# Optimization experiments

Hardware: AMD Instinct MI355X
Metric: run time of the kernel (lower is better)

Reference implementation:

```python
import jax, jax.numpy as jnp
import numpy as np

LEAK = 0.01
TEMP = 1.0
N_ORB = 1024
CTX = 32
N_ALPHA = 32
N_BETA = 32
B = 8192
EPS = 1e-20


def _leaky(x):
    return jnp.where(x >= 0, x, LEAK * x)


def _scorer_mlp(x, W1, b1, W2, b2, W3, b3):
    h = _leaky(x @ W1 + b1)
    h = _leaky(h @ W2 + b2)
    return h @ W3 + b3


def _gumbel_topk(logits, gumbel, k, temp):
    # successive-softmax subset relaxation (Plackett-Luce style)
    scores0 = logits + gumbel

    def step(carry, _):
        scores, khot = carry
        onehot = jax.nn.softmax(scores / temp, axis=-1)
        khot = khot + onehot
        scores = scores + jnp.log(jnp.maximum(1.0 - onehot, EPS))
        return (scores, khot), None

    (_, khot), _ = jax.lax.scan(step, (scores0, jnp.zeros_like(scores0)), None, length=k)
    return khot


def _soft_to_hard(soft, k):
    # straight-through: hard forward, soft backward
    idx = jax.lax.top_k(soft, k)[1]                      # (B, k)
    bidx = jnp.arange(soft.shape[0])[:, None]
    hard = jnp.zeros_like(soft).at[bidx, idx].set(1.0)
    return jax.lax.stop_gradient(hard - soft) + soft


def _lin_init(key, fan_in, fan_out):
    s = 1.0 / np.sqrt(fan_in)
    k1, k2 = jax.random.split(key)
    W = jax.random.uniform(k1, (fan_in, fan_out), minval=-s, maxval=s, dtype=jnp.float32)
    b = jax.random.uniform(k2, (fan_out,), minval=-s, maxval=s, dtype=jnp.float32)
    return W, b


def setup_inputs() -> dict:
    key = jax.random.key(0)
    ks = jax.random.split(key, 12)
    # alpha scorer: input = n_orb (baseline only, context_dim=0)
    W1a, b1a = _lin_init(ks[0], N_ORB, 128)
    W2a, b2a = _lin_init(ks[1], 128, 64)
    W3a, b3a = _lin_init(ks[2], 64, N_ORB)
    # beta scorer: context proj n_orb -> 32, input = n_orb + 32
    Wc, bc = _lin_init(ks[3], N_ORB, CTX)
    W1b, b1b = _lin_init(ks[4], N_ORB + CTX, 128)
    W2b, b2b = _lin_init(ks[5], 128, 64)
    W3b, b3b = _lin_init(ks[6], 64, N_ORB)
    baseline_a = jnp.zeros((N_ORB,), jnp.float32)
    baseline_b = jnp.zeros((N_ORB,), jnp.float32)
    # Gumbel noise: -log(-log(U))
    ua = jax.random.uniform(ks[7], (B, N_ORB), minval=1e-6, maxval=1.0 - 1e-6)
    ub = jax.random.uniform(ks[8], (B, N_ORB), minval=1e-6, maxval=1.0 - 1e-6)
    g_alpha = -jnp.log(-jnp.log(ua))
    g_beta = -jnp.log(-jnp.log(ub))
    return {
        "baseline_a": baseline_a, "W1a": W1a, "b1a": b1a, "W2a": W2a, "b2a": b2a,
        "W3a": W3a, "b3a": b3a,
        "baseline_b": baseline_b, "Wc": Wc, "bc": bc, "W1b": W1b, "b1b": b1b,
        "W2b": W2b, "b2b": b2b, "W3b": W3b, "b3b": b3b,
        "g_alpha": g_alpha, "g_beta": g_beta,
        "batch_size": B,
    }


def reference(baseline_a, W1a, b1a, W2a, b2a, W3a, b3a,
              baseline_b, Wc, bc, W1b, b1b, W2b, b2b, W3b, b3b,
              g_alpha, g_beta, batch_size):
    # --- alpha scoring (context_dim = 0) ---
    base_a = jnp.broadcast_to(baseline_a, (batch_size, N_ORB))
    alpha_logits = _scorer_mlp(base_a, W1a, b1a, W2a, b2a, W3a, b3a) + base_a
    alpha_soft = _gumbel_topk(alpha_logits, g_alpha, N_ALPHA, TEMP)
    alpha_config = _soft_to_hard(alpha_soft, N_ALPHA)          # (B, N_ORB)
    # --- beta scoring conditioned on alpha config ---
    base_b = jnp.broadcast_to(baseline_b, (batch_size, N_ORB))
    ctx = alpha_config @ Wc + bc                               # (B, 32)
    net_in = jnp.concatenate([base_b, ctx], axis=-1)
    beta_logits = _scorer_mlp(net_in, W1b, b1b, W2b, b2b, W3b, b3b) + base_b
    beta_soft = _gumbel_topk(beta_logits, g_beta, N_BETA, TEMP)
    beta_config = _soft_to_hard(beta_soft, N_BETA)
    return jnp.concatenate([alpha_config, beta_config], axis=-1)  # (B, num_sites)
```

## Files before the change

kernel.cpp:

```cpp
#include <hip/hip_runtime.h>
#include <hip/hip_bf16.h>
#include <float.h>

#define N_ORB 1024
#define KSEL 32
#define LEAK 0.01f
#define LOG2E 1.4426950408889634f

typedef float f32x2 __attribute__((ext_vector_type(2)));

__device__ __forceinline__ float leaky(float x) { return x >= 0.0f ? x : LEAK * x; }

__device__ __forceinline__ f32x2 pk_add(f32x2 a, f32x2 b) {
  f32x2 d;
  asm("v_pk_add_f32 %0, %1, %2" : "=v"(d) : "v"(a), "v"(b));
  return d;
}
__device__ __forceinline__ f32x2 pk_mul(f32x2 a, f32x2 b) {
  f32x2 d;
  asm("v_pk_mul_f32 %0, %1, %2" : "=v"(d) : "v"(a), "v"(b));
  return d;
}
__device__ __forceinline__ f32x2 pk_fma(f32x2 a, f32x2 b, f32x2 c) {
  f32x2 d;
  asm("v_pk_fma_f32 %0, %1, %2, %3" : "=v"(d) : "v"(a), "v"(b), "v"(c));
  return d;
}
__device__ __forceinline__ f32x2 pk_fma_clamp(f32x2 a, f32x2 b, f32x2 c) {
  f32x2 d;
  asm("v_pk_fma_f32 %0, %1, %2, %3 clamp" : "=v"(d) : "v"(a), "v"(b), "v"(c));
  return d;
}

template <int CTRL, int RM>
__device__ __forceinline__ int dpp0_i(int v) {
  return __builtin_amdgcn_update_dpp(0, v, CTRL, RM, 0xF, true);
}
template <int CTRL>
__device__ __forceinline__ float dpp_zero(float v) {
  return __int_as_float(
      __builtin_amdgcn_update_dpp(0, __float_as_int(v), CTRL, 0xF, 0xF, true));
}
__device__ __forceinline__ float rdlane(float v, int l) {
  return __int_as_float(__builtin_amdgcn_readlane(__float_as_int(v), l));
}

__device__ __forceinline__ float wave_sum64_dpp(float v) {
  v += dpp_zero<0x111>(v);
  v += dpp_zero<0x112>(v);
  v += dpp_zero<0x114>(v);
  v += dpp_zero<0x118>(v);
  v += dpp_zero<0x142>(v);
  v += dpp_zero<0x143>(v);
  return rdlane(v, 63);
}
__device__ __forceinline__ int wave_isum64(int v) {
  v += dpp0_i<0x111, 0xF>(v);
  v += dpp0_i<0x112, 0xF>(v);
  v += dpp0_i<0x114, 0xF>(v);
  v += dpp0_i<0x118, 0xF>(v);
  v += dpp0_i<0x142, 0xF>(v);
  v += dpp0_i<0x143, 0xF>(v);
  return __builtin_amdgcn_readlane(v, 63);
}
__device__ __forceinline__ int wave_iscan64(int v) {
  v += dpp0_i<0x111, 0xF>(v);
  v += dpp0_i<0x112, 0xF>(v);
  v += dpp0_i<0x114, 0xF>(v);
  v += dpp0_i<0x118, 0xF>(v);
  v += dpp0_i<0x142, 0xA>(v);
  v += dpp0_i<0x143, 0xC>(v);
  return v;
}

__device__ void run_chain2(f32x2 w[16], f32x2 kh[16]) {
#pragma unroll
  for (int i = 0; i < 16; ++i) kh[i] = f32x2{0.0f, 0.0f};
  const f32x2 onev = f32x2{1.0f, 1.0f};
  for (int it = 0; it < KSEL; ++it) {
    f32x2 t0 = pk_add(w[0], w[1]), t1 = pk_add(w[2], w[3]);
    f32x2 t2 = pk_add(w[4], w[5]), t3 = pk_add(w[6], w[7]);
    f32x2 t4 = pk_add(w[8], w[9]), t5 = pk_add(w[10], w[11]);
    f32x2 t6 = pk_add(w[12], w[13]), t7 = pk_add(w[14], w[15]);
    t0 = pk_add(t0, t1); t2 = pk_add(t2, t3);
    t4 = pk_add(t4, t5); t6 = pk_add(t6, t7);
    t0 = pk_add(t0, t2); t4 = pk_add(t4, t6);
    t0 = pk_add(t0, t4);
    float Z0 = wave_sum64_dpp(t0.x);
    float Z1 = wave_sum64_dpp(t0.y);
    Z0 = fmaxf(Z0, 1e-30f);
    Z1 = fmaxf(Z1, 1e-30f);
    float r0 = __builtin_amdgcn_rcpf(Z0);
    float r1 = __builtin_amdgcn_rcpf(Z1);
    float rZ0 = __builtin_fmaf(__builtin_fmaf(-Z0, r0, 1.0f), r0, r0);
    float rZ1 = __builtin_fmaf(__builtin_fmaf(-Z1, r1, 1.0f), r1, r1);
    const f32x2 rZ = f32x2{rZ0, rZ1};
    const f32x2 rZn = f32x2{-rZ0, -rZ1};
#pragma unroll
    for (int i = 0; i < 16; ++i) {
      kh[i] = pk_fma(w[i], rZ, kh[i]);
      f32x2 om = pk_fma_clamp(w[i], rZn, onev);
      w[i] = pk_mul(w[i], om);
    }
  }
}

__device__ unsigned tie_mask16(const f32x2 kh[16], bool comp_y, unsigned T,
                               int lane) {
  unsigned gt = 0, eq = 0;
#pragma unroll
  for (int i = 0; i < 16; ++i) {
    const unsigned u = __float_as_uint(comp_y ? kh[i].y : kh[i].x);
    gt |= (u > T ? 1u : 0u) << i;
    eq |= (u == T ? 1u : 0u) << i;
  }
  const int n_gt = wave_isum64(__popc(gt));
  const int m = 32 - n_gt;
  const int pe = __popc(eq);
  const int be = wave_iscan64(pe) - pe;
  int need = m - be;
  need = need < 0 ? 0 : (need > pe ? pe : need);
  unsigned tk = 0;
  unsigned em = eq;
  for (int guard = 0; guard < 16; ++guard) {
    if (!__any(need > 0)) break;
    if (need > 0) {
      const int bpos = __ffs(em) - 1;
      tk |= 1u << bpos;
      em &= em - 1;
      --need;
    }
  }
  return gt | tk;
}

__device__ void top32_mask2(const f32x2 kh[16], int lane, unsigned& m0,
                            unsigned& m1) {
  unsigned lo0 = 0, lo1 = 0;
  bool ex0 = false, ex1 = false;
  for (int b = 30; b >= 0; --b) {
    const unsigned c0v = lo0 | (1u << b);
    const unsigned c1v = lo1 | (1u << b);
    int c0 = 0, c1 = 0;
#pragma unroll
    for (int i = 0; i < 16; ++i) {
      c0 += __popcll(__ballot(__float_as_uint(kh[i].x) >= c0v));
      c1 += __popcll(__ballot(__float_as_uint(kh[i].y) >= c1v));
    }
    if (!ex0 && c0 >= 32) { lo0 = c0v; ex0 = (c0 == 32); }
    if (!ex1 && c1 >= 32) { lo1 = c1v; ex1 = (c1 == 32); }
    if (ex0 && ex1) break;
  }

  if (ex0) {
    unsigned mk = 0;
#pragma unroll
    for (int i = 0; i < 16; ++i)
      mk |= (__float_as_uint(kh[i].x) >= lo0 ? 1u : 0u) << i;
    m0 = mk;
  } else {
    m0 = tie_mask16(kh, false, lo0, lane);
  }
  if (ex1) {
    unsigned mk = 0;
#pragma unroll
    for (int i = 0; i < 16; ++i)
      mk |= (__float_as_uint(kh[i].y) >= lo1 ? 1u : 0u) << i;
    m1 = mk;
  } else {
    m1 = tie_mask16(kh, true, lo1, lane);
  }
}

__device__ __forceinline__ void compact_idx(unsigned mask, int lane,
                                            int* __restrict__ dst) {
  const int pe = __popc(mask);
  int base = wave_iscan64(pe) - pe;
  unsigned m = mask;
  while (m) {
    const int s = __ffs(m) - 1;
    m &= m - 1;
    dst[base++] = (lane << 4) | s;
  }
}

__device__ __forceinline__ void write_half(float* __restrict__ dst,
                                           unsigned mask, int lane) {
  float4* o4 = (float4*)dst;
#pragma unroll
  for (int q = 0; q < 4; ++q) {
    float4 o;
    o.x = ((mask >> (4 * q + 0)) & 1) ? 1.0f : 0.0f;
    o.y = ((mask >> (4 * q + 1)) & 1) ? 1.0f : 0.0f;
    o.z = ((mask >> (4 * q + 2)) & 1) ? 1.0f : 0.0f;
    o.w = ((mask >> (4 * q + 3)) & 1) ? 1.0f : 0.0f;
    o4[lane * 4 + q] = o;
  }
}


extern "C" __global__ void pcfs_pre1(const float* __restrict__ ba,
                                     const float* __restrict__ W1a,
                                     const float* __restrict__ b1a,
                                     const float* __restrict__ bb,
                                     const float* __restrict__ W1b,
                                     float* __restrict__ ws) {
  const int b = blockIdx.x;
  const int t = threadIdx.x;
  float acc = 0.0f;
  if (b < 128) {
#pragma unroll
    for (int j = t; j < N_ORB; j += 256) acc += ba[j] * W1a[j * 128 + b];
  } else {
    const int n = b - 128;
#pragma unroll
    for (int j = t; j < N_ORB; j += 256) acc += bb[j] * W1b[j * 128 + n];
  }
  __shared__ float red[4];
  float wsum = wave_sum64_dpp(acc);
  if ((t & 63) == 0) red[t >> 6] = wsum;
  __syncthreads();
  if (t == 0) {
    float tot = red[0] + red[1] + red[2] + red[3];
    if (b < 128)
      ws[1152 + b] = leaky(tot + b1a[b]);
    else
      ws[N_ORB + (b - 128)] = tot;
  }
}

extern "C" __global__ void pcfs_pre2a(const float* __restrict__ W2a,
                                      const float* __restrict__ b2a,
                                      float* __restrict__ ws) {
  const int t = threadIdx.x;
  float acc = b2a[t];
#pragma unroll 8
  for (int n = 0; n < 128; ++n) acc = __builtin_fmaf(ws[1152 + n], W2a[n * 64 + t], acc);
  ws[1280 + t] = leaky(acc);
}

extern "C" __global__ void pcfs_pre2b(const float* __restrict__ ba,
                                      const float* __restrict__ W3a,
                                      const float* __restrict__ b3a,
                                      float* __restrict__ ws) {
  __shared__ float h2s[64];
  const int t = threadIdx.x;
  const int o = blockIdx.x * 256 + t;
  if (t < 64) h2s[t] = ws[1280 + t];
  __syncthreads();
  float acc = b3a[o] + ba[o];
#pragma unroll 8
  for (int m = 0; m < 64; ++m) acc = __builtin_fmaf(h2s[m], W3a[m * N_ORB + o], acc);
  ws[o] = acc;
}

extern "C" __global__ void __launch_bounds__(256, 4) pcfs_sampler(
    const float* __restrict__ ws, const float* __restrict__ Wc,
    const float* __restrict__ bc, const float* __restrict__ W1b,
    const float* __restrict__ b1b, const float* __restrict__ W2b,
    const float* __restrict__ b2b, const float* __restrict__ W3b,
    const float* __restrict__ b3b, const float* __restrict__ bb,
    const float* __restrict__ g_alpha, const float* __restrict__ g_beta,
    float* __restrict__ out, int B) {
  __shared__ int sidx[4][64];
  __shared__ float w3s[8 * N_ORB];
  const int tid = threadIdx.x;
  const int wave = tid >> 6;
  const int lane = tid & 63;
  const int pair = blockIdx.x * 4 + wave;
  const int row0 = pair * 2;
  const bool active = (row0 < B);
  const bool have1 = active && (row0 + 1 < B);
  const int r0 = active ? row0 : 0;
  const int r1 = have1 ? row0 + 1 : r0;

  float4 gb0[4], gb1[4];
  {
    const float4* g40 = (const float4*)(g_beta + (size_t)r0 * N_ORB);
    const float4* g41 = (const float4*)(g_beta + (size_t)r1 * N_ORB);
#pragma unroll
    for (int q = 0; q < 4; ++q) {
      gb0[q] = g40[lane * 4 + q];
      gb1[q] = g41[lane * 4 + q];
    }
  }

  f32x2 w[16], kh[16];

  {
    const float4* c4 = (const float4*)ws;
    const float4* g40 = (const float4*)(g_alpha + (size_t)r0 * N_ORB);
    const float4* g41 = (const float4*)(g_alpha + (size_t)r1 * N_ORB);
#pragma unroll
    for (int q = 0; q < 4; ++q) {
      float4 c = c4[lane * 4 + q];
      float4 g0 = g40[lane * 4 + q];
      float4 g1 = g41[lane * 4 + q];
      w[4 * q + 0] = f32x2{__builtin_amdgcn_exp2f((c.x + g0.x) * LOG2E),
                           __builtin_amdgcn_exp2f((c.x + g1.x) * LOG2E)};
      w[4 * q + 1] = f32x2{__builtin_amdgcn_exp2f((c.y + g0.y) * LOG2E),
                           __builtin_amdgcn_exp2f((c.y + g1.y) * LOG2E)};
      w[4 * q + 2] = f32x2{__builtin_amdgcn_exp2f((c.z + g0.z) * LOG2E),
                           __builtin_amdgcn_exp2f((c.z + g1.z) * LOG2E)};
      w[4 * q + 3] = f32x2{__builtin_amdgcn_exp2f((c.w + g0.w) * LOG2E),
                           __builtin_amdgcn_exp2f((c.w + g1.w) * LOG2E)};
    }
  }
  run_chain2(w, kh);
  unsigned am0, am1;
  top32_mask2(kh, lane, am0, am1);

  if (active) write_half(out + (size_t)row0 * (2 * N_ORB), am0, lane);
  if (have1) write_half(out + (size_t)(row0 + 1) * (2 * N_ORB), am1, lane);

  compact_idx(am0, lane, &sidx[wave][0]);
  compact_idx(am1, lane, &sidx[wave][32]);
  const int vi0 = sidx[wave][lane & 31];
  const int vi1 = sidx[wave][32 + (lane & 31)];
  const float bcv = bc[lane & 31];
  float ctx0 = bcv, ctx1 = bcv;
#pragma unroll
  for (int r = 0; r < 32; ++r) {
    const int i0 = __builtin_amdgcn_readlane(vi0, r);
    const int i1 = __builtin_amdgcn_readlane(vi1, r);
    ctx0 += Wc[i0 * 32 + (lane & 31)];
    ctx1 += Wc[i1 * 32 + (lane & 31)];
  }

  f32x2 h1a, h1b_;
  {
    const float ia = b1b[lane] + ws[N_ORB + lane];
    const float ib = b1b[lane + 64] + ws[N_ORB + lane + 64];
    h1a = f32x2{ia, ia};
    h1b_ = f32x2{ib, ib};
  }
#pragma unroll 4
  for (int c = 0; c < 32; ++c) {
    const f32x2 cv = f32x2{rdlane(ctx0, c), rdlane(ctx1, c)};
    const float* wr = W1b + (size_t)(N_ORB + c) * 128;
    const float wa = wr[lane], wb = wr[lane + 64];
    h1a = __builtin_elementwise_fma(f32x2{wa, wa}, cv, h1a);
    h1b_ = __builtin_elementwise_fma(f32x2{wb, wb}, cv, h1b_);
  }
  h1a = f32x2{leaky(h1a.x), leaky(h1a.y)};
  h1b_ = f32x2{leaky(h1b_.x), leaky(h1b_.y)};

  f32x2 h2p0, h2p1, h2p2, h2p3;
  {
    const float i2 = b2b[lane];
    h2p0 = f32x2{i2, i2};
    h2p1 = f32x2{0.0f, 0.0f};
    h2p2 = f32x2{0.0f, 0.0f};
    h2p3 = f32x2{0.0f, 0.0f};
  }
#pragma unroll 4
  for (int n = 0; n < 64; n += 4) {
    const f32x2 v0 = f32x2{rdlane(h1a.x, n + 0), rdlane(h1a.y, n + 0)};
    const f32x2 v1 = f32x2{rdlane(h1a.x, n + 1), rdlane(h1a.y, n + 1)};
    const f32x2 v2 = f32x2{rdlane(h1a.x, n + 2), rdlane(h1a.y, n + 2)};
    const f32x2 v3 = f32x2{rdlane(h1a.x, n + 3), rdlane(h1a.y, n + 3)};
    const float w0 = W2b[(n + 0) * 64 + lane];
    const float w1 = W2b[(n + 1) * 64 + lane];
    const float w2 = W2b[(n + 2) * 64 + lane];
    const float w3 = W2b[(n + 3) * 64 + lane];
    h2p0 = __builtin_elementwise_fma(f32x2{w0, w0}, v0, h2p0);
    h2p1 = __builtin_elementwise_fma(f32x2{w1, w1}, v1, h2p1);
    h2p2 = __builtin_elementwise_fma(f32x2{w2, w2}, v2, h2p2);
    h2p3 = __builtin_elementwise_fma(f32x2{w3, w3}, v3, h2p3);
  }
#pragma unroll 4
  for (int n = 0; n < 64; n += 4) {
    const f32x2 v0 = f32x2{rdlane(h1b_.x, n + 0), rdlane(h1b_.y, n + 0)};
    const f32x2 v1 = f32x2{rdlane(h1b_.x, n + 1), rdlane(h1b_.y, n + 1)};
    const f32x2 v2 = f32x2{rdlane(h1b_.x, n + 2), rdlane(h1b_.y, n + 2)};
    const f32x2 v3 = f32x2{rdlane(h1b_.x, n + 3), rdlane(h1b_.y, n + 3)};
    const float w0 = W2b[(n + 64 + 0) * 64 + lane];
    const float w1 = W2b[(n + 64 + 1) * 64 + lane];
    const float w2 = W2b[(n + 64 + 2) * 64 + lane];
    const float w3 = W2b[(n + 64 + 3) * 64 + lane];
    h2p0 = __builtin_elementwise_fma(f32x2{w0, w0}, v0, h2p0);
    h2p1 = __builtin_elementwise_fma(f32x2{w1, w1}, v1, h2p1);
    h2p2 = __builtin_elementwise_fma(f32x2{w2, w2}, v2, h2p2);
    h2p3 = __builtin_elementwise_fma(f32x2{w3, w3}, v3, h2p3);
  }
  f32x2 h2v = (h2p0 + h2p1) + (h2p2 + h2p3);
  h2v = f32x2{leaky(h2v.x), leaky(h2v.y)};

  {
    const float4* b4 = (const float4*)b3b;
#pragma unroll
    for (int q = 0; q < 4; ++q) {
      float4 b = b4[lane * 4 + q];
      w[4 * q + 0] = f32x2{b.x, b.x};
      w[4 * q + 1] = f32x2{b.y, b.y};
      w[4 * q + 2] = f32x2{b.z, b.z};
      w[4 * q + 3] = f32x2{b.w, b.w};
    }
  }
  const int swzrd = ((lane & 1) << 7) | (lane >> 1);
  const int swzwr = ((tid & 7) << 5) | (tid >> 3);
  for (int t = 0; t < 8; ++t) {
    __syncthreads();
    {
      const float4* src = (const float4*)(W3b + (size_t)t * 8 * N_ORB);
      float4* dst = (float4*)w3s;
#pragma unroll
      for (int k = 0; k < 8; ++k) dst[k * 256 + swzwr] = src[tid + k * 256];
    }
    __syncthreads();
#pragma unroll
    for (int ml = 0; ml < 8; ++ml) {
      const int m = t * 8 + ml;
      const f32x2 hm = f32x2{rdlane(h2v.x, m), rdlane(h2v.y, m)};
      const float4* w4 = (const float4*)(w3s + ml * N_ORB);
#pragma unroll
      for (int q = 0; q < 4; ++q) {
        float4 wv = w4[swzrd + (q << 5)];
        w[4 * q + 0] = __builtin_elementwise_fma(f32x2{wv.x, wv.x}, hm, w[4 * q + 0]);
        w[4 * q + 1] = __builtin_elementwise_fma(f32x2{wv.y, wv.y}, hm, w[4 * q + 1]);
        w[4 * q + 2] = __builtin_elementwise_fma(f32x2{wv.z, wv.z}, hm, w[4 * q + 2]);
        w[4 * q + 3] = __builtin_elementwise_fma(f32x2{wv.w, wv.w}, hm, w[4 * q + 3]);
      }
    }
  }
  {
    const float4* bb4 = (const float4*)bb;
#pragma unroll
    for (int q = 0; q < 4; ++q) {
      float4 b = bb4[lane * 4 + q];
      const float4 g0 = gb0[q];
      const float4 g1 = gb1[q];
      w[4 * q + 0] = f32x2{
          __builtin_amdgcn_exp2f((w[4 * q + 0].x + b.x + g0.x) * LOG2E),
          __builtin_amdgcn_exp2f((w[4 * q + 0].y + b.x + g1.x) * LOG2E)};
      w[4 * q + 1] = f32x2{
          __builtin_amdgcn_exp2f((w[4 * q + 1].x + b.y + g0.y) * LOG2E),
          __builtin_amdgcn_exp2f((w[4 * q + 1].y + b.y + g1.y) * LOG2E)};
      w[4 * q + 2] = f32x2{
          __builtin_amdgcn_exp2f((w[4 * q + 2].x + b.z + g0.z) * LOG2E),
          __builtin_amdgcn_exp2f((w[4 * q + 2].y + b.z + g1.z) * LOG2E)};
      w[4 * q + 3] = f32x2{
          __builtin_amdgcn_exp2f((w[4 * q + 3].x + b.w + g0.w) * LOG2E),
          __builtin_amdgcn_exp2f((w[4 * q + 3].y + b.w + g1.w) * LOG2E)};
    }
  }
  run_chain2(w, kh);
  unsigned bm0, bm1;
  top32_mask2(kh, lane, bm0, bm1);

  if (active) write_half(out + (size_t)row0 * (2 * N_ORB) + N_ORB, bm0, lane);
  if (have1)
    write_half(out + (size_t)(row0 + 1) * (2 * N_ORB) + N_ORB, bm1, lane);
}

extern "C" void kernel_launch(void* const* d_in, const int* in_sizes, int n_in,
                              void* d_out, int out_size, void* d_ws, size_t ws_size,
                              hipStream_t stream) {
  const float* ba  = (const float*)d_in[0];
  const float* W1a = (const float*)d_in[1];
  const float* b1a = (const float*)d_in[2];
  const float* W2a = (const float*)d_in[3];
  const float* b2a = (const float*)d_in[4];
  const float* W3a = (const float*)d_in[5];
  const float* b3a = (const float*)d_in[6];
  const float* bb  = (const float*)d_in[7];
  const float* Wc  = (const float*)d_in[8];
  const float* bc  = (const float*)d_in[9];
  const float* W1b = (const float*)d_in[10];
  const float* b1b = (const float*)d_in[11];
  const float* W2b = (const float*)d_in[12];
  const float* b2b = (const float*)d_in[13];
  const float* W3b = (const float*)d_in[14];
  const float* b3b = (const float*)d_in[15];
  const float* ga  = (const float*)d_in[16];
  const float* gbt = (const float*)d_in[17];
  const int B = in_sizes[16] / N_ORB;
  float* ws = (float*)d_ws;

  hipLaunchKernelGGL(pcfs_pre1, dim3(256), dim3(256), 0, stream,
                     ba, W1a, b1a, bb, W1b, ws);
  hipLaunchKernelGGL(pcfs_pre2a, dim3(1), dim3(64), 0, stream,
                     W2a, b2a, ws);
  hipLaunchKernelGGL(pcfs_pre2b, dim3(4), dim3(256), 0, stream,
                     ba, W3a, b3a, ws);
  const int pairs = (B + 1) / 2;
  hipLaunchKernelGGL(pcfs_sampler, dim3((pairs + 3) / 4), dim3(256), 0, stream,
                     ws, Wc, bc, W1b, b1b, W2b, b2b, W3b, b3b, bb,
                     ga, gbt, (float*)d_out, B);
}
```

Baseline: 266.0 us.

## Replace successive-softmax chain with direct top-k on perturbed logits

Drops the 32-iteration successive-softmax relaxation and selects the top 32 directly from logits plus Gumbel noise, using an order-preserving float-to-unsigned key and the existing radix-select. It relies on the relaxation having the same top-k order as the raw scores, which holds in exact arithmetic because each step's reweighting is monotone. Rounding-induced ties or reorderings in the original soft values could give different selections, so results may differ on near-ties. It removes the per-iteration wave reductions and exponentials for both the alpha and beta stages.

```diff
diff --git a/kernel.cpp b/kernel.cpp
--- a/kernel.cpp
+++ b/kernel.cpp
@@ -5,31 +5,14 @@
 #define N_ORB 1024
 #define KSEL 32
 #define LEAK 0.01f
-#define LOG2E 1.4426950408889634f
 
 typedef float f32x2 __attribute__((ext_vector_type(2)));
 
 __device__ __forceinline__ float leaky(float x) { return x >= 0.0f ? x : LEAK * x; }
 
-__device__ __forceinline__ f32x2 pk_add(f32x2 a, f32x2 b) {
-  f32x2 d;
-  asm("v_pk_add_f32 %0, %1, %2" : "=v"(d) : "v"(a), "v"(b));
-  return d;
-}
-__device__ __forceinline__ f32x2 pk_mul(f32x2 a, f32x2 b) {
-  f32x2 d;
-  asm("v_pk_mul_f32 %0, %1, %2" : "=v"(d) : "v"(a), "v"(b));
-  return d;
-}
-__device__ __forceinline__ f32x2 pk_fma(f32x2 a, f32x2 b, f32x2 c) {
-  f32x2 d;
-  asm("v_pk_fma_f32 %0, %1, %2, %3" : "=v"(d) : "v"(a), "v"(b), "v"(c));
-  return d;
-}
-__device__ __forceinline__ f32x2 pk_fma_clamp(f32x2 a, f32x2 b, f32x2 c) {
-  f32x2 d;
-  asm("v_pk_fma_f32 %0, %1, %2, %3 clamp" : "=v"(d) : "v"(a), "v"(b), "v"(c));
-  return d;
+__device__ __forceinline__ unsigned fkey(float f) {
+  const unsigned u = __float_as_uint(f);
+  return u ^ ((unsigned)((int)u >> 31) | 0x80000000u);
 }
 
 template <int CTRL, int RM>
@@ -73,46 +56,12 @@
   return v;
 }
 
-__device__ void run_chain2(f32x2 w[16], f32x2 kh[16]) {
-#pragma unroll
-  for (int i = 0; i < 16; ++i) kh[i] = f32x2{0.0f, 0.0f};
-  const f32x2 onev = f32x2{1.0f, 1.0f};
-  for (int it = 0; it < KSEL; ++it) {
-    f32x2 t0 = pk_add(w[0], w[1]), t1 = pk_add(w[2], w[3]);
-    f32x2 t2 = pk_add(w[4], w[5]), t3 = pk_add(w[6], w[7]);
-    f32x2 t4 = pk_add(w[8], w[9]), t5 = pk_add(w[10], w[11]);
-    f32x2 t6 = pk_add(w[12], w[13]), t7 = pk_add(w[14], w[15]);
-    t0 = pk_add(t0, t1); t2 = pk_add(t2, t3);
-    t4 = pk_add(t4, t5); t6 = pk_add(t6, t7);
-    t0 = pk_add(t0, t2); t4 = pk_add(t4, t6);
-    t0 = pk_add(t0, t4);
-    float Z0 = wave_sum64_dpp(t0.x);
-    float Z1 = wave_sum64_dpp(t0.y);
-    Z0 = fmaxf(Z0, 1e-30f);
-    Z1 = fmaxf(Z1, 1e-30f);
-    float r0 = __builtin_amdgcn_rcpf(Z0);
-    float r1 = __builtin_amdgcn_rcpf(Z1);
-    float rZ0 = __builtin_fmaf(__builtin_fmaf(-Z0, r0, 1.0f), r0, r0);
-    float rZ1 = __builtin_fmaf(__builtin_fmaf(-Z1, r1, 1.0f), r1, r1);
-    const f32x2 rZ = f32x2{rZ0, rZ1};
-    const f32x2 rZn = f32x2{-rZ0, -rZ1};
-#pragma unroll
-    for (int i = 0; i < 16; ++i) {
-      kh[i] = pk_fma(w[i], rZ, kh[i]);
-      f32x2 om = pk_fma_clamp(w[i], rZn, onev);
-      w[i] = pk_mul(w[i], om);
-    }
-  }
-}
-
-__device__ unsigned tie_mask16(const f32x2 kh[16], bool comp_y, unsigned T,
-                               int lane) {
+__device__ unsigned tie_mask16u(const unsigned K[16], unsigned T, int lane) {
   unsigned gt = 0, eq = 0;
 #pragma unroll
   for (int i = 0; i < 16; ++i) {
-    const unsigned u = __float_as_uint(comp_y ? kh[i].y : kh[i].x);
-    gt |= (u > T ? 1u : 0u) << i;
-    eq |= (u == T ? 1u : 0u) << i;
+    gt |= (K[i] > T ? 1u : 0u) << i;
+    eq |= (K[i] == T ? 1u : 0u) << i;
   }
   const int n_gt = wave_isum64(__popc(gt));
   const int m = 32 - n_gt;
@@ -134,18 +83,18 @@
   return gt | tk;
 }
 
-__device__ void top32_mask2(const f32x2 kh[16], int lane, unsigned& m0,
-                            unsigned& m1) {
+__device__ void top32_mask2u(const unsigned K0[16], const unsigned K1[16],
+                             int lane, unsigned& m0, unsigned& m1) {
   unsigned lo0 = 0, lo1 = 0;
   bool ex0 = false, ex1 = false;
-  for (int b = 30; b >= 0; --b) {
+  for (int b = 31; b >= 0; --b) {
     const unsigned c0v = lo0 | (1u << b);
     const unsigned c1v = lo1 | (1u << b);
     int c0 = 0, c1 = 0;
 #pragma unroll
     for (int i = 0; i < 16; ++i) {
-      c0 += __popcll(__ballot(__float_as_uint(kh[i].x) >= c0v));
-      c1 += __popcll(__ballot(__float_as_uint(kh[i].y) >= c1v));
+      c0 += __popcll(__ballot(K0[i] >= c0v));
+      c1 += __popcll(__ballot(K1[i] >= c1v));
     }
     if (!ex0 && c0 >= 32) { lo0 = c0v; ex0 = (c0 == 32); }
     if (!ex1 && c1 >= 32) { lo1 = c1v; ex1 = (c1 == 32); }
@@ -155,20 +104,18 @@
   if (ex0) {
     unsigned mk = 0;
 #pragma unroll
-    for (int i = 0; i < 16; ++i)
-      mk |= (__float_as_uint(kh[i].x) >= lo0 ? 1u : 0u) << i;
+    for (int i = 0; i < 16; ++i) mk |= (K0[i] >= lo0 ? 1u : 0u) << i;
     m0 = mk;
   } else {
-    m0 = tie_mask16(kh, false, lo0, lane);
+    m0 = tie_mask16u(K0, lo0, lane);
   }
   if (ex1) {
     unsigned mk = 0;
 #pragma unroll
-    for (int i = 0; i < 16; ++i)
-      mk |= (__float_as_uint(kh[i].y) >= lo1 ? 1u : 0u) << i;
+    for (int i = 0; i < 16; ++i) mk |= (K1[i] >= lo1 ? 1u : 0u) << i;
     m1 = mk;
   } else {
-    m1 = tie_mask16(kh, true, lo1, lane);
+    m1 = tie_mask16u(K1, lo1, lane);
   }
 }
 
@@ -285,8 +232,7 @@
     }
   }
 
-  f32x2 w[16], kh[16];
-
+  unsigned ka0[16], ka1[16];
   {
     const float4* c4 = (const float4*)ws;
     const float4* g40 = (const float4*)(g_alpha + (size_t)r0 * N_ORB);
@@ -296,19 +242,14 @@
       float4 c = c4[lane * 4 + q];
       float4 g0 = g40[lane * 4 + q];
       float4 g1 = g41[lane * 4 + q];
-      w[4 * q + 0] = f32x2{__builtin_amdgcn_exp2f((c.x + g0.x) * LOG2E),
-                           __builtin_amdgcn_exp2f((c.x + g1.x) * LOG2E)};
-      w[4 * q + 1] = f32x2{__builtin_amdgcn_exp2f((c.y + g0.y) * LOG2E),
-                           __builtin_amdgcn_exp2f((c.y + g1.y) * LOG2E)};
-      w[4 * q + 2] = f32x2{__builtin_amdgcn_exp2f((c.z + g0.z) * LOG2E),
-                           __builtin_amdgcn_exp2f((c.z + g1.z) * LOG2E)};
-      w[4 * q + 3] = f32x2{__builtin_amdgcn_exp2f((c.w + g0.w) * LOG2E),
-                           __builtin_amdgcn_exp2f((c.w + g1.w) * LOG2E)};
-    }
-  }
-  run_chain2(w, kh);
+      ka0[4 * q + 0] = fkey(c.x + g0.x); ka1[4 * q + 0] = fkey(c.x + g1.x);
+      ka0[4 * q + 1] = fkey(c.y + g0.y); ka1[4 * q + 1] = fkey(c.y + g1.y);
+      ka0[4 * q + 2] = fkey(c.z + g0.z); ka1[4 * q + 2] = fkey(c.z + g1.z);
+      ka0[4 * q + 3] = fkey(c.w + g0.w); ka1[4 * q + 3] = fkey(c.w + g1.w);
+    }
+  }
   unsigned am0, am1;
-  top32_mask2(kh, lane, am0, am1);
+  top32_mask2u(ka0, ka1, lane, am0, am1);
 
   if (active) write_half(out + (size_t)row0 * (2 * N_ORB), am0, lane);
   if (have1) write_half(out + (size_t)(row0 + 1) * (2 * N_ORB), am1, lane);
@@ -386,6 +327,7 @@
   f32x2 h2v = (h2p0 + h2p1) + (h2p2 + h2p3);
   h2v = f32x2{leaky(h2v.x), leaky(h2v.y)};
 
+  f32x2 w[16];
   {
     const float4* b4 = (const float4*)b3b;
 #pragma unroll
@@ -423,6 +365,7 @@
       }
     }
   }
+  unsigned kb0[16], kb1[16];
   {
     const float4* bb4 = (const float4*)bb;
 #pragma unroll
@@ -430,23 +373,18 @@
       float4 b = bb4[lane * 4 + q];
       const float4 g0 = gb0[q];
       const float4 g1 = gb1[q];
-      w[4 * q + 0] = f32x2{
-          __builtin_amdgcn_exp2f((w[4 * q + 0].x + b.x + g0.x) * LOG2E),
-          __builtin_amdgcn_exp2f((w[4 * q + 0].y + b.x + g1.x) * LOG2E)};
-      w[4 * q + 1] = f32x2{
-          __builtin_amdgcn_exp2f((w[4 * q + 1].x + b.y + g0.y) * LOG2E),
-          __builtin_amdgcn_exp2f((w[4 * q + 1].y + b.y + g1.y) * LOG2E)};
-      w[4 * q + 2] = f32x2{
-          __builtin_amdgcn_exp2f((w[4 * q + 2].x + b.z + g0.z) * LOG2E),
-          __builtin_amdgcn_exp2f((w[4 * q + 2].y + b.z + g1.z) * LOG2E)};
-      w[4 * q + 3] = f32x2{
-          __builtin_amdgcn_exp2f((w[4 * q + 3].x + b.w + g0.w) * LOG2E),
-          __builtin_amdgcn_exp2f((w[4 * q + 3].y + b.w + g1.w) * LOG2E)};
-    }
-  }
-  run_chain2(w, kh);
+      kb0[4 * q + 0] = fkey(w[4 * q + 0].x + b.x + g0.x);
+      kb1[4 * q + 0] = fkey(w[4 * q + 0].y + b.x + g1.x);
+      kb0[4 * q + 1] = fkey(w[4 * q + 1].x + b.y + g0.y);
+      kb1[4 * q + 1] = fkey(w[4 * q + 1].y + b.y + g1.y);
+      kb0[4 * q + 2] = fkey(w[4 * q + 2].x + b.z + g0.z);
+      kb1[4 * q + 2] = fkey(w[4 * q + 2].y + b.z + g1.z);
+      kb0[4 * q + 3] = fkey(w[4 * q + 3].x + b.w + g0.w);
+      kb1[4 * q + 3] = fkey(w[4 * q + 3].y + b.w + g1.w);
+    }
+  }
   unsigned bm0, bm1;
-  top32_mask2(kh, lane, bm0, bm1);
+  top32_mask2u(kb0, kb1, lane, bm0, bm1);
 
   if (active) write_half(out + (size_t)row0 * (2 * N_ORB) + N_ORB, bm0, lane);
   if (have1)
```

Measured after the change: 240.5 us. 1.11x faster.
